# Kernel tuning notes

Measured on AMD Instinct MI355X. Metric: run time of the kernel, lower is better.

## Reference

```python
import jax, jax.numpy as jnp
import numpy as np

# Dims: B batch, T target seq, S source seq (self-attn: S==T), V symmetry-rep dim (D4 -> 8),
# M heads-per-group, K groups (num_heads = M*K = 8), F head_rep dim (TrivialRep -> 1),
# Hqk qk head width, Hv v head width, C feature width per rep component.
B, T, S, V, M, K, F, Hqk, Hv, C = 4, 512, 512, 8, 2, 4, 1, 32, 32, 256


def setup_inputs() -> dict:
    key = jax.random.key(0)
    ks = jax.random.split(key, 6)
    x = jax.random.normal(ks[0], (B, T, V, C), jnp.float32)
    # SymDecompLinear kernels: q has extra out reps (F, M, K); k/v have (F, 1, K) -> m axis broadcast
    Wq = jax.random.normal(ks[1], (C, M, K, F, Hqk), jnp.float32) / np.sqrt(C).astype(np.float32)
    Wk = jax.random.normal(ks[2], (C, K, F, Hqk), jnp.float32) / np.sqrt(C).astype(np.float32)
    Wv = jax.random.normal(ks[3], (C, K, F, Hv), jnp.float32) / np.sqrt(C).astype(np.float32)
    # out projection contracts the (M, K, F, Hv) head structure back to C features
    Wout = jax.random.normal(ks[4], (M, K, F, Hv, C), jnp.float32) / np.sqrt(M * K * F * Hv).astype(np.float32)
    mask = jax.random.bernoulli(ks[5], 0.9, (B, T, S))
    mask = mask.at[..., 0].set(True)  # guarantee each query attends to >=1 key
    return dict(x=x, Wq=Wq, Wk=Wk, Wv=Wv, Wout=Wout, mask=mask)


def reference(x, Wq, Wk, Wv, Wout, mask):
    # projections: q -> [B,T,V,M,K,F,Hqk]; k,v -> [B,S,V,K,F,H] (single head per group, broadcast over m)
    q = jnp.einsum('btvc,cmkfh->btvmkfh', x, Wq)
    k = jnp.einsum('bsvc,ckfh->bsvkfh', x, Wk)
    v = jnp.einsum('bsvc,ckfh->bsvkfh', x, Wv)
    scale = 1.0 / np.sqrt(F * Hqk).astype(np.float32)
    # logits retain the symmetry axis v: [B,T,S,V,M,K]
    logits = scale * jnp.einsum('btvmkfh,bsvkfh->btsvmk', q, k)
    lgmsk = mask[..., :, :, None, None, None]  # [B,T,S,1,1,1]
    weight = jax.nn.softmax(logits, axis=-4, where=lgmsk)  # softmax over source axis s
    att = jnp.einsum('btsvmk,bsvkfh->btvmkfh', weight, v)
    out = jnp.einsum('btvmkfh,mkfhc->btvc', att, Wout)
    return out
```

## Files before the change

### kernel.cpp

```cpp
#include <hip/hip_runtime.h>
#include <hip/hip_bf16.h>
#include <cstdint>

#define BB 4
#define TT 512
#define SS 512
#define VV 8
#define NROWS (BB * TT * VV)


typedef __attribute__((ext_vector_type(8))) short bf16x8;
typedef __attribute__((ext_vector_type(4))) float f32x4;

static __device__ __forceinline__ short f2bf(float f) {
  union { float f; unsigned u; } x; x.f = f;
  unsigned r = x.u + 0x7FFFu + ((x.u >> 16) & 1u);
  return (short)(r >> 16);
}

static __device__ __forceinline__ unsigned cvt_pk(float lo, float hi) {
  unsigned r;
  asm("v_cvt_pk_bf16_f32 %0, %1, %2" : "=v"(r) : "v"(lo), "v"(hi));
  return r;
}

static __device__ __forceinline__ void gload_lds16(const void* g, void* l) {
  __builtin_amdgcn_global_load_lds(
      (const __attribute__((address_space(1))) void*)g,
      (__attribute__((address_space(3))) void*)l, 16, 0, 0);
}

__global__ __launch_bounds__(256) void pack_all_kernel(const float* __restrict__ Wq,
                                                       const float* __restrict__ Wk,
                                                       const float* __restrict__ Wv,
                                                       const float* __restrict__ Wout,
                                                       const int* __restrict__ mask,
                                                       short* __restrict__ WcatT,
                                                       short* __restrict__ WoutT,
                                                       unsigned long long* __restrict__ mask64) {
  if (blockIdx.x < 768) {
    int idx = blockIdx.x * 256 + threadIdx.x;
    const float qscale = 0.17677669529663687f * 1.4426950408889634f;
    if (idx < 512 * 256) {
      int n = idx >> 8, c = idx & 255;
      float val;
      if (n < 256)      val = Wq[c * 256 + n] * qscale;
      else if (n < 384) val = Wk[c * 128 + (n - 256)];
      else              val = Wv[c * 128 + (n - 384)];
      WcatT[idx] = f2bf(val);
    } else {
      int j = idx - 512 * 256;
      int cc = j >> 8, jj = j & 255;
      WoutT[j] = f2bf(Wout[jj * 256 + cc]);
    }
  } else {
    int row = (blockIdx.x - 768) * 4 + (threadIdx.x >> 6);
    int ln = threadIdx.x & 63;
    const int* mrow = mask + (size_t)row * SS;
#pragma unroll
    for (int c = 0; c < 8; ++c) {
      unsigned long long bal = __ballot(mrow[c * 64 + ln] != 0);
      if (ln == 0) mask64[(size_t)row * 8 + c] = bal;
    }
  }
}

template <int N, bool AF32, int EPI>
__global__ __launch_bounds__(256) void gemm_bf16(const void* __restrict__ Ap,
                                                 const short* __restrict__ Bt,
                                                 void* __restrict__ Cout,
                                                 short* __restrict__ Vt2) {
  __shared__ short As[64][64];
  __shared__ short Bs[128][64];
  const int tid = threadIdx.x;
  const int w = tid >> 6, ln = tid & 63;
  const int wr = (w >> 1) * 32, wc = (w & 1) * 64;
  const int bm = blockIdx.x * 64, bn = blockIdx.y * 128;
  const int lr = ln & 15, lk = (ln >> 4) * 8;
  const int r0 = tid >> 3, ko = (tid & 7) * 8;

  f32x4 acc[2][4] = {};

  for (int k0 = 0; k0 < 256; k0 += 64) {
    bf16x8 a[2];
    if constexpr (AF32) {
#pragma unroll
      for (int i = 0; i < 2; ++i) {
        size_t row = (size_t)(bm + i * 32 + r0);
        const float* Af = (const float*)Ap;
        float4 f0 = *(const float4*)&Af[row * 256 + k0 + ko];
        float4 f1 = *(const float4*)&Af[row * 256 + k0 + ko + 4];
        uint4 pk = make_uint4(cvt_pk(f0.x, f0.y), cvt_pk(f0.z, f0.w),
                              cvt_pk(f1.x, f1.y), cvt_pk(f1.z, f1.w));
        a[i] = *(bf16x8*)&pk;
      }
    }
    __syncthreads();
#pragma unroll
    for (int i = 0; i < 4; ++i)
      gload_lds16(&Bt[(size_t)(bn + i * 32 + r0) * 256 + k0 + ko],
                  &Bs[i * 32 + r0][ko]);
    if constexpr (AF32) {
#pragma unroll
      for (int i = 0; i < 2; ++i) *(bf16x8*)&As[i * 32 + r0][ko] = a[i];
    } else {
#pragma unroll
      for (int i = 0; i < 2; ++i)
        gload_lds16(&((const short*)Ap)[(size_t)(bm + i * 32 + r0) * 256 + k0 + ko],
                    &As[i * 32 + r0][ko]);
    }
    __syncthreads();

#pragma unroll
    for (int kk = 0; kk < 2; ++kk) {
      bf16x8 af[2], bfr[4];
#pragma unroll
      for (int mi = 0; mi < 2; ++mi)
        af[mi] = *(const bf16x8*)&As[wr + mi * 16 + lr][kk * 32 + lk];
#pragma unroll
      for (int ni = 0; ni < 4; ++ni)
        bfr[ni] = *(const bf16x8*)&Bs[wc + ni * 16 + lr][kk * 32 + lk];
#pragma unroll
      for (int mi = 0; mi < 2; ++mi)
#pragma unroll
        for (int ni = 0; ni < 4; ++ni)
          acc[mi][ni] = __builtin_amdgcn_mfma_f32_16x16x32_bf16(af[mi], bfr[ni], acc[mi][ni], 0, 0, 0);
    }
  }

  const int rowg = (ln >> 4) * 4;
  if constexpr (EPI == 0) {
#pragma unroll
    for (int mi = 0; mi < 2; ++mi)
#pragma unroll
      for (int r = 0; r < 4; ++r) {
        size_t row = bm + wr + mi * 16 + rowg + r;
#pragma unroll
        for (int ni = 0; ni < 4; ++ni)
          ((float*)Cout)[row * N + bn + wc + ni * 16 + lr] = acc[mi][ni][r];
      }
  } else {
    int slotN[4], h16[4];
#pragma unroll
    for (int ni = 0; ni < 4; ++ni) {
      int jb = bn + wc + ni * 16;
      slotN[ni] = jb >> 5;
      h16[ni] = jb & 16;
    }
    short* q16 = (short*)Cout;
#pragma unroll
    for (int mi = 0; mi < 2; ++mi)
#pragma unroll
      for (int r = 0; r < 4; ++r) {
        int row = bm + wr + mi * 16 + rowg + r;
        int t = (row >> 3) & 511;
        int bv = (row >> 12) * 8 + (row & 7);
        unsigned u0 = cvt_pk(acc[mi][0][r], acc[mi][1][r]);
        unsigned u1 = cvt_pk(acc[mi][2][r], acc[mi][3][r]);
        short vals[4] = {(short)u0, (short)(u0 >> 16), (short)u1, (short)(u1 >> 16)};
#pragma unroll
        for (int ni = 0; ni < 4; ++ni) {
          int slot = slotN[ni], h = h16[ni] + lr;
          if (slot < 12) {
            q16[((size_t)bv << 18) + slot * 16384 + t * 32 + h] = vals[ni];
          } else {
            Vt2[(((size_t)bv * 4 + (slot - 12)) << 14) + ((t >> 6) << 11) + (h << 6) + (t & 63)] = vals[ni];
          }
        }
      }
  }
}

__global__ __launch_bounds__(256) void attn_mfma(const short* __restrict__ qkvh,
                                                 const short* __restrict__ Vt2,
                                                 const unsigned long long* __restrict__ mask64,
                                                 short* __restrict__ att) {
  const int orig = blockIdx.x;
  const int widx = (orig & 7) * 128 + (orig >> 3);
  const int head = widx >> 3;
  const int t0 = (widx & 7) * 64;
  const int bv = head >> 2;
  const int b  = bv >> 3;
  const int v  = bv & 7;
  const int k  = head & 3;
  const int tid = threadIdx.x;
  const int w  = tid >> 6;
  const int ln = tid & 63;
  const int gq = ln >> 4;
  const int tr = ln & 15;

  __shared__ __align__(16) short Pt[4][16][72];

  bf16x8 qf[2];
  {
    const short* qp = qkvh + ((size_t)(bv * 16 + k) * 512 + (t0 + w * 16 + tr)) * 32 + gq * 8;
    qf[0] = *(const bf16x8*)qp;
    qf[1] = *(const bf16x8*)(qp + 4 * 512 * 32);
  }

  f32x4 acc_o[2][2] = {};
  float l_run[2] = {0.f, 0.f};

  const short* kb = qkvh + (size_t)(bv * 16 + 8 + k) * 16384 + gq * 8;
  const short* vb = Vt2 + (size_t)(bv * 4 + k) * 16384 + tr * 64 + gq * 8;
  const unsigned long long* mrow = mask64 + ((size_t)(b * TT + t0 + w * 16 + tr)) * 8;

  bf16x8 kf[4], vf[2][2];
  unsigned long long mb;
#pragma unroll
  for (int st = 0; st < 4; ++st)
    kf[st] = *(const bf16x8*)(kb + (size_t)(st * 16 + tr) * 32);
#pragma unroll
  for (int sh = 0; sh < 2; ++sh)
#pragma unroll
    for (int hh = 0; hh < 2; ++hh)
      vf[sh][hh] = *(const bf16x8*)(vb + hh * 16 * 64 + sh * 32);
  mb = mrow[0];

  for (int c = 0; c < 8; ++c) {
    bf16x8 kn[4], vn[2][2];
    unsigned long long mbn;
    if (c < 7) {
#pragma unroll
      for (int st = 0; st < 4; ++st)
        kn[st] = *(const bf16x8*)(kb + (size_t)((c + 1) * 64 + st * 16 + tr) * 32);
#pragma unroll
      for (int sh = 0; sh < 2; ++sh)
#pragma unroll
        for (int hh = 0; hh < 2; ++hh)
          vn[sh][hh] = *(const bf16x8*)(vb + (c + 1) * 2048 + hh * 16 * 64 + sh * 32);
      mbn = mrow[c + 1];
    }

    unsigned mlo = (unsigned)mb, mhi = (unsigned)(mb >> 32);
    float bias[4][4];
#pragma unroll
    for (int st = 0; st < 4; ++st) {
      unsigned wbits = (st < 2) ? mlo : mhi;
      const int base = (st & 1) * 16 + 4 * gq;
#pragma unroll
      for (int r = 0; r < 4; ++r)
        bias[st][r] = ((wbits >> (base + r)) & 1u) ? 0.f : -INFINITY;
    }

#pragma unroll
    for (int m = 0; m < 2; ++m) {
      f32x4 lac[4];
#pragma unroll
      for (int st = 0; st < 4; ++st) {
        f32x4 z = {0.f, 0.f, 0.f, 0.f};
        lac[st] = __builtin_amdgcn_mfma_f32_16x16x32_bf16(kf[st], qf[m], z, 0, 0, 0);
      }
      float pl[4][4];
      float rs = 0.f;
#pragma unroll
      for (int st = 0; st < 4; ++st)
#pragma unroll
        for (int r = 0; r < 4; ++r) {
          pl[st][r] = __builtin_amdgcn_exp2f(lac[st][r] + bias[st][r]);
          rs += pl[st][r];
        }
      rs += __shfl_xor(rs, 16);
      rs += __shfl_xor(rs, 32);
      l_run[m] += rs;

#pragma unroll
      for (int st = 0; st < 4; ++st)
        *(uint2*)&Pt[w][tr][st * 16 + 4 * gq] =
            make_uint2(cvt_pk(pl[st][0], pl[st][1]), cvt_pk(pl[st][2], pl[st][3]));
#pragma unroll
      for (int sh = 0; sh < 2; ++sh) {
        bf16x8 pf = *(const bf16x8*)&Pt[w][tr][sh * 32 + gq * 8];
#pragma unroll
        for (int hh = 0; hh < 2; ++hh)
          acc_o[m][hh] = __builtin_amdgcn_mfma_f32_16x16x32_bf16(pf, vf[sh][hh], acc_o[m][hh], 0, 0, 0);
      }
    }

    if (c < 7) {
#pragma unroll
      for (int st = 0; st < 4; ++st) kf[st] = kn[st];
#pragma unroll
      for (int sh = 0; sh < 2; ++sh)
#pragma unroll
        for (int hh = 0; hh < 2; ++hh) vf[sh][hh] = vn[sh][hh];
      mb = mbn;
    }
  }

#pragma unroll
  for (int m = 0; m < 2; ++m) {
    float invR[4];
#pragma unroll
    for (int r = 0; r < 4; ++r) invR[r] = 1.f / __shfl(l_run[m], 4 * gq + r);
#pragma unroll
    for (int r = 0; r < 4; ++r) {
      short* dst = att + ((size_t)((b * TT + t0 + w * 16 + 4 * gq + r) * VV + v)) * 256
                 + m * 128 + k * 32 + tr;
      unsigned u = cvt_pk(acc_o[m][0][r] * invR[r], acc_o[m][1][r] * invR[r]);
      dst[0]  = (short)u;
      dst[16] = (short)(u >> 16);
    }
  }
}

extern "C" void kernel_launch(void* const* d_in, const int* in_sizes, int n_in,
                              void* d_out, int out_size, void* d_ws, size_t ws_size,
                              hipStream_t stream) {
  const float* x = (const float*)d_in[0];
  const float* Wq = (const float*)d_in[1];
  const float* Wk = (const float*)d_in[2];
  const float* Wv = (const float*)d_in[3];
  const float* Wout = (const float*)d_in[4];
  const int* mask = (const int*)d_in[5];
  float* out = (float*)d_out;

  short* WcatT = (short*)d_ws;
  short* WoutT = WcatT + 512 * 256;
  short* qkvh  = WoutT + 256 * 256;
  short* att   = qkvh + (size_t)NROWS * 512;
  short* Vt2   = att + (size_t)NROWS * 256;
  unsigned long long* mask64 = (unsigned long long*)(Vt2 + (size_t)128 * 16384);

  pack_all_kernel<<<768 + 512, 256, 0, stream>>>(Wq, Wk, Wv, Wout, mask, WcatT, WoutT, mask64);
  gemm_bf16<512, true, 2><<<dim3(NROWS / 64, 4), 256, 0, stream>>>(x, WcatT, qkvh, Vt2);
  attn_mfma<<<1024, 256, 0, stream>>>(qkvh, Vt2, mask64, att);
  gemm_bf16<256, false, 0><<<dim3(NROWS / 64, 2), 256, 0, stream>>>(att, WoutT, out, nullptr);
}
```

Baseline: 66.01 us.

## Split attention over two source halves and merge partials in output GEMM

Attention blocks now each handle half of the source sequence, doubling the grid from 1024 to 2048 blocks. Each block writes unnormalized partial outputs and per-row softmax denominators to workspace. The output-projection GEMM combines the two halves, sums the denominators and normalizes while loading A. This targets better occupancy and shorter per-block serial loops in the attention kernel, at the cost of extra workspace traffic and heavier A loading in the final GEMM. Merging is only correct without a running max, i.e. when the two halves share the same exponent reference.

```diff
diff --git a/kernel.cpp b/kernel.cpp
--- a/kernel.cpp
+++ b/kernel.cpp
@@ -16,6 +16,11 @@
   union { float f; unsigned u; } x; x.f = f;
   unsigned r = x.u + 0x7FFFu + ((x.u >> 16) & 1u);
   return (short)(r >> 16);
+}
+
+static __device__ __forceinline__ float bf2f(short s) {
+  union { unsigned u; float f; } t; t.u = ((unsigned)(unsigned short)s) << 16;
+  return t.f;
 }
 
 static __device__ __forceinline__ unsigned cvt_pk(float lo, float hi) {
@@ -65,11 +70,12 @@
   }
 }
 
-template <int N, bool AF32, int EPI>
+template <int N, int AMODE, int EPI>
 __global__ __launch_bounds__(256) void gemm_bf16(const void* __restrict__ Ap,
                                                  const short* __restrict__ Bt,
                                                  void* __restrict__ Cout,
-                                                 short* __restrict__ Vt2) {
+                                                 short* __restrict__ Vt2,
+                                                 const float* __restrict__ lbuf) {
   __shared__ short As[64][64];
   __shared__ short Bs[128][64];
   const int tid = threadIdx.x;
@@ -83,7 +89,7 @@
 
   for (int k0 = 0; k0 < 256; k0 += 64) {
     bf16x8 a[2];
-    if constexpr (AF32) {
+    if constexpr (AMODE == 1) {
 #pragma unroll
       for (int i = 0; i < 2; ++i) {
         size_t row = (size_t)(bm + i * 32 + r0);
@@ -94,21 +100,32 @@
                               cvt_pk(f1.x, f1.y), cvt_pk(f1.z, f1.w));
         a[i] = *(bf16x8*)&pk;
       }
+    } else if constexpr (AMODE == 2) {
+      const short* Op = (const short*)Ap;
+#pragma unroll
+      for (int i = 0; i < 2; ++i) {
+        size_t row = (size_t)(bm + i * 32 + r0);
+        int j8 = k0 + ko;
+        int slot = j8 >> 5;
+        bf16x8 o1 = *(const bf16x8*)&Op[row * 256 + j8];
+        bf16x8 o2 = *(const bf16x8*)&Op[((size_t)NROWS + row) * 256 + j8];
+        float l = lbuf[row * 8 + slot] + lbuf[((size_t)NROWS + row) * 8 + slot];
+        float rl = 1.0f / l;
+        unsigned pk[4];
+#pragma unroll
+        for (int e = 0; e < 4; ++e)
+          pk[e] = cvt_pk((bf2f(o1[2 * e]) + bf2f(o2[2 * e])) * rl,
+                         (bf2f(o1[2 * e + 1]) + bf2f(o2[2 * e + 1])) * rl);
+        a[i] = *(bf16x8*)&pk;
+      }
     }
     __syncthreads();
 #pragma unroll
     for (int i = 0; i < 4; ++i)
       gload_lds16(&Bt[(size_t)(bn + i * 32 + r0) * 256 + k0 + ko],
                   &Bs[i * 32 + r0][ko]);
-    if constexpr (AF32) {
-#pragma unroll
-      for (int i = 0; i < 2; ++i) *(bf16x8*)&As[i * 32 + r0][ko] = a[i];
-    } else {
-#pragma unroll
-      for (int i = 0; i < 2; ++i)
-        gload_lds16(&((const short*)Ap)[(size_t)(bm + i * 32 + r0) * 256 + k0 + ko],
-                    &As[i * 32 + r0][ko]);
-    }
+#pragma unroll
+    for (int i = 0; i < 2; ++i) *(bf16x8*)&As[i * 32 + r0][ko] = a[i];
     __syncthreads();
 
 #pragma unroll
@@ -174,11 +191,15 @@
 __global__ __launch_bounds__(256) void attn_mfma(const short* __restrict__ qkvh,
                                                  const short* __restrict__ Vt2,
                                                  const unsigned long long* __restrict__ mask64,
-                                                 short* __restrict__ att) {
+                                                 short* __restrict__ Op,
+                                                 float* __restrict__ lbuf) {
   const int orig = blockIdx.x;
-  const int widx = (orig & 7) * 128 + (orig >> 3);
-  const int head = widx >> 3;
-  const int t0 = (widx & 7) * 64;
+  const int widx = (orig & 7) * 256 + (orig >> 3);
+  const int head = widx >> 4;
+  const int rem = widx & 15;
+  const int t0 = (rem >> 1) * 64;
+  const int shalf = rem & 1;
+  const int sbase = shalf * 256;
   const int bv = head >> 2;
   const int b  = bv >> 3;
   const int v  = bv & 7;
@@ -201,9 +222,9 @@
   f32x4 acc_o[2][2] = {};
   float l_run[2] = {0.f, 0.f};
 
-  const short* kb = qkvh + (size_t)(bv * 16 + 8 + k) * 16384 + gq * 8;
-  const short* vb = Vt2 + (size_t)(bv * 4 + k) * 16384 + tr * 64 + gq * 8;
-  const unsigned long long* mrow = mask64 + ((size_t)(b * TT + t0 + w * 16 + tr)) * 8;
+  const short* kb = qkvh + (size_t)(bv * 16 + 8 + k) * 16384 + (size_t)sbase * 32 + gq * 8;
+  const short* vb = Vt2 + (size_t)(bv * 4 + k) * 16384 + (sbase >> 6) * 2048 + tr * 64 + gq * 8;
+  const unsigned long long* mrow = mask64 + ((size_t)(b * TT + t0 + w * 16 + tr)) * 8 + (sbase >> 6);
 
   bf16x8 kf[4], vf[2][2];
   unsigned long long mb;
@@ -217,10 +238,10 @@
       vf[sh][hh] = *(const bf16x8*)(vb + hh * 16 * 64 + sh * 32);
   mb = mrow[0];
 
-  for (int c = 0; c < 8; ++c) {
+  for (int c = 0; c < 4; ++c) {
     bf16x8 kn[4], vn[2][2];
     unsigned long long mbn;
-    if (c < 7) {
+    if (c < 3) {
 #pragma unroll
       for (int st = 0; st < 4; ++st)
         kn[st] = *(const bf16x8*)(kb + (size_t)((c + 1) * 64 + st * 16 + tr) * 32);
@@ -277,7 +298,7 @@
       }
     }
 
-    if (c < 7) {
+    if (c < 3) {
 #pragma unroll
       for (int st = 0; st < 4; ++st) kf[st] = kn[st];
 #pragma unroll
@@ -290,17 +311,19 @@
 
 #pragma unroll
   for (int m = 0; m < 2; ++m) {
-    float invR[4];
-#pragma unroll
-    for (int r = 0; r < 4; ++r) invR[r] = 1.f / __shfl(l_run[m], 4 * gq + r);
 #pragma unroll
     for (int r = 0; r < 4; ++r) {
-      short* dst = att + ((size_t)((b * TT + t0 + w * 16 + 4 * gq + r) * VV + v)) * 256
-                 + m * 128 + k * 32 + tr;
-      unsigned u = cvt_pk(acc_o[m][0][r] * invR[r], acc_o[m][1][r] * invR[r]);
+      size_t row = (size_t)(b * TT + t0 + w * 16 + 4 * gq + r) * VV + v;
+      short* dst = Op + ((size_t)shalf * NROWS + row) * 256 + m * 128 + k * 32 + tr;
+      unsigned u = cvt_pk(acc_o[m][0][r], acc_o[m][1][r]);
       dst[0]  = (short)u;
       dst[16] = (short)(u >> 16);
     }
+  }
+  if (gq == 0) {
+    size_t row = (size_t)(b * TT + t0 + w * 16 + tr) * VV + v;
+    lbuf[((size_t)shalf * NROWS + row) * 8 + k]     = l_run[0];
+    lbuf[((size_t)shalf * NROWS + row) * 8 + 4 + k] = l_run[1];
   }
 }
 
@@ -318,12 +341,13 @@
   short* WcatT = (short*)d_ws;
   short* WoutT = WcatT + 512 * 256;
   short* qkvh  = WoutT + 256 * 256;
-  short* att   = qkvh + (size_t)NROWS * 512;
-  short* Vt2   = att + (size_t)NROWS * 256;
-  unsigned long long* mask64 = (unsigned long long*)(Vt2 + (size_t)128 * 16384);
+  short* Op    = qkvh + (size_t)NROWS * 512;
+  short* Vt2   = Op + (size_t)2 * NROWS * 256;
+  float* lbuf  = (float*)(Vt2 + (size_t)128 * 16384);
+  unsigned long long* mask64 = (unsigned long long*)(lbuf + (size_t)2 * NROWS * 8);
 
   pack_all_kernel<<<768 + 512, 256, 0, stream>>>(Wq, Wk, Wv, Wout, mask, WcatT, WoutT, mask64);
-  gemm_bf16<512, true, 2><<<dim3(NROWS / 64, 4), 256, 0, stream>>>(x, WcatT, qkvh, Vt2);
-  attn_mfma<<<1024, 256, 0, stream>>>(qkvh, Vt2, mask64, att);
-  gemm_bf16<256, false, 0><<<dim3(NROWS / 64, 2), 256, 0, stream>>>(att, WoutT, out, nullptr);
-}
+  gemm_bf16<512, 1, 2><<<dim3(NROWS / 64, 4), 256, 0, stream>>>(x, WcatT, qkvh, Vt2, nullptr);
+  attn_mfma<<<2048, 256, 0, stream>>>(qkvh, Vt2, mask64, Op, lbuf);
+  gemm_bf16<256, 2, 0><<<dim3(NROWS / 64, 2), 256, 0, stream>>>(Op, WoutT, out, nullptr, lbuf);
+}
```

Result: slower. 70.88 us (+7.4%).
